# Kernel optimization log

Hardware: AMD Instinct MI355X
Metric: run time of the kernel (lower is better)

The kernel has to match this reference:

```python
import jax, jax.numpy as jnp
import numpy as np

TOKENS, IN_F, OUT_F = 65536, 1024, 1024


def setup_inputs() -> dict:
    key = jax.random.key(0)
    kx, kw = jax.random.split(key)
    x = jax.random.normal(kx, (TOKENS, IN_F), dtype=jnp.float32)
    weight = jax.random.normal(kw, (OUT_F, IN_F), dtype=jnp.float32) * 0.05
    return {"x": x, "weight": weight}


def reference(x, weight):
    # per-output-row scale: alpha = mean(|w|) over in_features
    alpha = jnp.mean(jnp.abs(weight), axis=1, keepdims=True)  # [out, 1]
    w_bin = jnp.sign(weight) * alpha                          # [out, in]
    # F.linear(x, w_bin) == x @ w_bin.T
    return jnp.einsum("ti,oi->to", x, w_bin)
```

## Files before the change

### kernel.cpp

```cpp
#include <hip/hip_runtime.h>


typedef _Float16 half8 __attribute__((ext_vector_type(8)));
typedef _Float16 half4v __attribute__((ext_vector_type(4)));
typedef float f32x4 __attribute__((ext_vector_type(4)));

#define TOKENS 65536
#define INF 1024
#define OUTF 1024
#define BM 256
#define BN 256
#define BK 32
#define NKT 32

__device__ __forceinline__ void gload_lds16(const void* g, void* l) {
  __builtin_amdgcn_global_load_lds(
      (const __attribute__((address_space(1))) unsigned int*)g,
      (__attribute__((address_space(3))) unsigned int*)l, 16, 0, 0);
}

__device__ __forceinline__ half8 cvt8(f32x4 a, f32x4 b) {
  half8 h;
  h[0] = (_Float16)a[0]; h[1] = (_Float16)a[1];
  h[2] = (_Float16)a[2]; h[3] = (_Float16)a[3];
  h[4] = (_Float16)b[0]; h[5] = (_Float16)b[1];
  h[6] = (_Float16)b[2]; h[7] = (_Float16)b[3];
  return h;
}

__global__ __launch_bounds__(256) void bl_prep(const float* __restrict__ w,
                                               _Float16* __restrict__ sbin,
                                               float* __restrict__ alpha) {
  const int o = blockIdx.x;
  const int tid = threadIdx.x;
  const float4 v = ((const float4*)(w + (size_t)o * INF))[tid];
  float s = fabsf(v.x) + fabsf(v.y) + fabsf(v.z) + fabsf(v.w);
  half4v h;
  h[0] = (_Float16)((v.x > 0.f) ? 1.f : ((v.x < 0.f) ? -1.f : 0.f));
  h[1] = (_Float16)((v.y > 0.f) ? 1.f : ((v.y < 0.f) ? -1.f : 0.f));
  h[2] = (_Float16)((v.z > 0.f) ? 1.f : ((v.z < 0.f) ? -1.f : 0.f));
  h[3] = (_Float16)((v.w > 0.f) ? 1.f : ((v.w < 0.f) ? -1.f : 0.f));
  *(half4v*)(sbin + (size_t)o * INF + tid * 4) = h;
#pragma unroll
  for (int off = 32; off > 0; off >>= 1) s += __shfl_down(s, off, 64);
  __shared__ float red[4];
  const int wave = tid >> 6, lane = tid & 63;
  if (lane == 0) red[wave] = s;
  __syncthreads();
  if (tid == 0) alpha[o] = (red[0] + red[1] + red[2] + red[3]) * (1.0f / 1024.0f);
}

__global__ __launch_bounds__(512, 2) void bl_gemm(const float* __restrict__ x,
                                                  const _Float16* __restrict__ sbin,
                                                  const float* __restrict__ alpha,
                                                  float* __restrict__ out) {
  __shared__ float ldsA[3][BM * BK];
  __shared__ _Float16 ldsB[3][BN * BK];

  const int tid = threadIdx.x;
  const int lane = tid & 63;
  const int wid = tid >> 6;
  const int l15 = lane & 15;
  const int kc = lane >> 4;
  const int wr = wid >> 1;
  const int wc = wid & 1;

  const int bid = blockIdx.x;
  const int wgid = (bid & 7) * 128 + (bid >> 3);
  const int bm0 = (wgid >> 2) * BM;
  const int bn0 = (wgid & 3) * BN;

  size_t aSrc[4];
  int aDst[4];
#pragma unroll
  for (int q = 0; q < 4; ++q) {
    const int ci = q * 512 + tid;
    const int row = ci >> 3;
    const int c = (ci & 7) ^ (row & 7);
    aSrc[q] = (size_t)(bm0 + row) * INF + c * 4;
    aDst[q] = ci * 16;
  }
  size_t bSrc[2];
  int bDst[2];
#pragma unroll
  for (int p = 0; p < 2; ++p) {
    const int ci = p * 512 + tid;
    const int row = ci >> 2;
    const int c = (ci & 3) ^ (row & 3);
    bSrc[p] = (size_t)(bn0 + row) * INF + c * 8;
    bDst[p] = ci * 16;
  }
  int aRd[4][2];
#pragma unroll
  for (int mf = 0; mf < 4; ++mf) {
    const int row = wr * 64 + mf * 16 + l15;
#pragma unroll
    for (int d = 0; d < 2; ++d)
      aRd[mf][d] = row * 128 + (((2 * kc + d) ^ (row & 7)) << 4);
  }
  int bRd[8];
#pragma unroll
  for (int nf = 0; nf < 8; ++nf) {
    const int row = wc * 128 + nf * 16 + l15;
    bRd[nf] = row * 64 + ((kc ^ (row & 3)) << 4);
  }

  f32x4 acc[4][8] = {};

#define STAGE(SB_, tk_)                                                        \
  {                                                                            \
    const size_t ko_ = (size_t)(tk_) * BK;                                     \
    gload_lds16(x + aSrc[0] + ko_, (char*)&ldsA[SB_][0] + aDst[0]);            \
    gload_lds16(x + aSrc[1] + ko_, (char*)&ldsA[SB_][0] + aDst[1]);            \
    gload_lds16(x + aSrc[2] + ko_, (char*)&ldsA[SB_][0] + aDst[2]);            \
    gload_lds16(x + aSrc[3] + ko_, (char*)&ldsA[SB_][0] + aDst[3]);            \
    gload_lds16(sbin + bSrc[0] + ko_, (char*)&ldsB[SB_][0] + bDst[0]);         \
    gload_lds16(sbin + bSrc[1] + ko_, (char*)&ldsB[SB_][0] + bDst[1]);         \
  }

#define COMPUTE(RB_)                                                           \
  {                                                                            \
    const char* pa_ = (const char*)&ldsA[RB_][0];                              \
    const char* pb_ = (const char*)&ldsB[RB_][0];                              \
    f32x4 lo0 = *(const f32x4*)(pa_ + aRd[0][0]);                              \
    f32x4 hi0 = *(const f32x4*)(pa_ + aRd[0][1]);                              \
    f32x4 lo1 = *(const f32x4*)(pa_ + aRd[1][0]);                              \
    f32x4 hi1 = *(const f32x4*)(pa_ + aRd[1][1]);                              \
    f32x4 lo2 = *(const f32x4*)(pa_ + aRd[2][0]);                              \
    f32x4 hi2 = *(const f32x4*)(pa_ + aRd[2][1]);                              \
    f32x4 lo3 = *(const f32x4*)(pa_ + aRd[3][0]);                              \
    f32x4 hi3 = *(const f32x4*)(pa_ + aRd[3][1]);                              \
    const half8 af0 = cvt8(lo0, hi0);                                          \
    const half8 af1 = cvt8(lo1, hi1);                                          \
    const half8 af2 = cvt8(lo2, hi2);                                          \
    const half8 af3 = cvt8(lo3, hi3);                                          \
    __builtin_amdgcn_s_setprio(1);                                             \
    _Pragma("unroll") for (int nf = 0; nf < 8; ++nf) {                         \
      const half8 b = *(const half8*)(pb_ + bRd[nf]);                          \
      acc[0][nf] = __builtin_amdgcn_mfma_f32_16x16x32_f16(af0, b, acc[0][nf], 0, 0, 0); \
      acc[1][nf] = __builtin_amdgcn_mfma_f32_16x16x32_f16(af1, b, acc[1][nf], 0, 0, 0); \
      acc[2][nf] = __builtin_amdgcn_mfma_f32_16x16x32_f16(af2, b, acc[2][nf], 0, 0, 0); \
      acc[3][nf] = __builtin_amdgcn_mfma_f32_16x16x32_f16(af3, b, acc[3][nf], 0, 0, 0); \
    }                                                                          \
    __builtin_amdgcn_s_setprio(0);                                             \
  }

#define PH(T_, RB_, SB_)                                                       \
  {                                                                            \
    STAGE(SB_, (T_) + 2);                                                      \
    COMPUTE(RB_);                                                              \
    asm volatile("s_waitcnt vmcnt(6)" ::: "memory");                           \
    __builtin_amdgcn_s_barrier();                                              \
  }

  STAGE(0, 0);
  STAGE(1, 1);
  asm volatile("s_waitcnt vmcnt(6)" ::: "memory");
  __builtin_amdgcn_s_barrier();

#pragma unroll 1
  for (int u = 0; u < 10; ++u) {
    PH(3 * u + 0, 0, 2)
    PH(3 * u + 1, 1, 0)
    PH(3 * u + 2, 2, 1)
  }
  COMPUTE(0);
  asm volatile("s_waitcnt vmcnt(0)" ::: "memory");
  __builtin_amdgcn_s_barrier();
  COMPUTE(1);

#undef PH
#undef COMPUTE
#undef STAGE

  float al[8];
#pragma unroll
  for (int n = 0; n < 8; ++n) al[n] = alpha[bn0 + wc * 128 + n * 16 + l15];
#pragma unroll
  for (int mf = 0; mf < 4; ++mf) {
    const int row0 = bm0 + wr * 64 + mf * 16 + kc * 4;
#pragma unroll
    for (int n = 0; n < 8; ++n) {
      const int col = bn0 + wc * 128 + n * 16 + l15;
#pragma unroll
      for (int j = 0; j < 4; ++j)
        out[(size_t)(row0 + j) * OUTF + col] = acc[mf][n][j] * al[n];
    }
  }
}

extern "C" void kernel_launch(void* const* d_in, const int* in_sizes, int n_in,
                              void* d_out, int out_size, void* d_ws, size_t ws_size,
                              hipStream_t stream) {
  const float* x = (const float*)d_in[0];
  const float* w = (const float*)d_in[1];
  float* out = (float*)d_out;
  _Float16* sbin = (_Float16*)d_ws;
  float* alpha = (float*)((char*)d_ws + (size_t)OUTF * INF * 2);

  bl_prep<<<dim3(OUTF), dim3(256), 0, stream>>>(w, sbin, alpha);
  bl_gemm<<<dim3((TOKENS / BM) * (OUTF / BN)), dim3(512), 0, stream>>>(x, sbin, alpha, out);
}
```

Measured before the change: 229.2 us.

## Pre-convert activations to fp16 in a separate pass and use fp16 GEMM

Adds a conversion kernel that writes x as fp16 into the workspace, then runs a new GEMM reading fp16 tiles with BK=64 and double buffering, removing per-tile fp32-to-fp16 conversion and halving LDS traffic for A. Falls back to a reworked fp32-input GEMM (two-stage buffering, adjusted B swizzle) when the workspace is too small. The extra pass adds a full read and write of the activation matrix through HBM.

```diff
diff --git a/kernel.cpp b/kernel.cpp
--- a/kernel.cpp
+++ b/kernel.cpp
@@ -10,8 +10,6 @@
 #define OUTF 1024
 #define BM 256
 #define BN 256
-#define BK 32
-#define NKT 32
 
 __device__ __forceinline__ void gload_lds16(const void* g, void* l) {
   __builtin_amdgcn_global_load_lds(
@@ -50,12 +48,23 @@
   if (tid == 0) alpha[o] = (red[0] + red[1] + red[2] + red[3]) * (1.0f / 1024.0f);
 }
 
-__global__ __launch_bounds__(512, 2) void bl_gemm(const float* __restrict__ x,
-                                                  const _Float16* __restrict__ sbin,
-                                                  const float* __restrict__ alpha,
-                                                  float* __restrict__ out) {
-  __shared__ float ldsA[3][BM * BK];
-  __shared__ _Float16 ldsB[3][BN * BK];
+__global__ __launch_bounds__(256) void bl_cvt(const float* __restrict__ x,
+                                              _Float16* __restrict__ x16) {
+  const size_t stride = (size_t)gridDim.x * 256 * 8;
+  for (size_t i = ((size_t)blockIdx.x * 256 + threadIdx.x) * 8;
+       i < (size_t)TOKENS * INF; i += stride) {
+    f32x4 v0 = *(const f32x4*)(x + i);
+    f32x4 v1 = *(const f32x4*)(x + i + 4);
+    *(half8*)(x16 + i) = cvt8(v0, v1);
+  }
+}
+
+__global__ __launch_bounds__(512) void bl_gemm16(const _Float16* __restrict__ x16,
+                                                 const _Float16* __restrict__ sbin,
+                                                 const float* __restrict__ alpha,
+                                                 float* __restrict__ out) {
+  __shared__ _Float16 ldsA[2][BM * 64];
+  __shared__ _Float16 ldsB[2][BN * 64];
 
   const int tid = threadIdx.x;
   const int lane = tid & 63;
@@ -70,24 +79,146 @@
   const int bm0 = (wgid >> 2) * BM;
   const int bn0 = (wgid & 3) * BN;
 
-  size_t aSrc[4];
-  int aDst[4];
+  int aSrc[4], bSrc[4];
+  int dst[4];
 #pragma unroll
   for (int q = 0; q < 4; ++q) {
     const int ci = q * 512 + tid;
     const int row = ci >> 3;
     const int c = (ci & 7) ^ (row & 7);
-    aSrc[q] = (size_t)(bm0 + row) * INF + c * 4;
+    aSrc[q] = (bm0 + row) * INF + c * 8;
+    bSrc[q] = (bn0 + row) * INF + c * 8;
+    dst[q] = ci * 16;
+  }
+  int slotKs[2];
+#pragma unroll
+  for (int ks = 0; ks < 2; ++ks) slotKs[ks] = (((ks * 4 + kc) ^ (l15 & 7)) << 4);
+  int aRd[4];
+#pragma unroll
+  for (int mf = 0; mf < 4; ++mf) aRd[mf] = (wr * 64 + mf * 16 + l15) * 128;
+  int bRd[8];
+#pragma unroll
+  for (int nf = 0; nf < 8; ++nf) bRd[nf] = (wc * 128 + nf * 16 + l15) * 128;
+
+  f32x4 acc[4][8] = {};
+
+#define STAGE(SB_, tk_)                                                        \
+  {                                                                            \
+    const int ko_ = (tk_)*64;                                                  \
+    gload_lds16(x16 + aSrc[0] + ko_, (char*)&ldsA[SB_][0] + dst[0]);           \
+    gload_lds16(x16 + aSrc[1] + ko_, (char*)&ldsA[SB_][0] + dst[1]);           \
+    gload_lds16(x16 + aSrc[2] + ko_, (char*)&ldsA[SB_][0] + dst[2]);           \
+    gload_lds16(x16 + aSrc[3] + ko_, (char*)&ldsA[SB_][0] + dst[3]);           \
+    gload_lds16(sbin + bSrc[0] + ko_, (char*)&ldsB[SB_][0] + dst[0]);          \
+    gload_lds16(sbin + bSrc[1] + ko_, (char*)&ldsB[SB_][0] + dst[1]);          \
+    gload_lds16(sbin + bSrc[2] + ko_, (char*)&ldsB[SB_][0] + dst[2]);          \
+    gload_lds16(sbin + bSrc[3] + ko_, (char*)&ldsB[SB_][0] + dst[3]);          \
+  }
+
+#define MF4(AC_, B_)                                                           \
+  acc[0][AC_] = __builtin_amdgcn_mfma_f32_16x16x32_f16(af0, B_, acc[0][AC_], 0, 0, 0); \
+  acc[1][AC_] = __builtin_amdgcn_mfma_f32_16x16x32_f16(af1, B_, acc[1][AC_], 0, 0, 0); \
+  acc[2][AC_] = __builtin_amdgcn_mfma_f32_16x16x32_f16(af2, B_, acc[2][AC_], 0, 0, 0); \
+  acc[3][AC_] = __builtin_amdgcn_mfma_f32_16x16x32_f16(af3, B_, acc[3][AC_], 0, 0, 0);
+
+#define KSLICE(RB_, KS_)                                                       \
+  {                                                                            \
+    const char* pa_ = (const char*)&ldsA[RB_][0];                              \
+    const char* pb_ = (const char*)&ldsB[RB_][0];                              \
+    const int sl_ = slotKs[KS_];                                               \
+    const half8 af0 = *(const half8*)(pa_ + aRd[0] + sl_);                     \
+    const half8 af1 = *(const half8*)(pa_ + aRd[1] + sl_);                     \
+    const half8 af2 = *(const half8*)(pa_ + aRd[2] + sl_);                     \
+    const half8 af3 = *(const half8*)(pa_ + aRd[3] + sl_);                     \
+    half8 b0 = *(const half8*)(pb_ + bRd[0] + sl_);                            \
+    half8 b1 = *(const half8*)(pb_ + bRd[1] + sl_);                            \
+    half8 b2 = *(const half8*)(pb_ + bRd[2] + sl_);                            \
+    half8 b3 = *(const half8*)(pb_ + bRd[3] + sl_);                            \
+    MF4(0, b0) MF4(1, b1) MF4(2, b2) MF4(3, b3)                                \
+    b0 = *(const half8*)(pb_ + bRd[4] + sl_);                                  \
+    b1 = *(const half8*)(pb_ + bRd[5] + sl_);                                  \
+    b2 = *(const half8*)(pb_ + bRd[6] + sl_);                                  \
+    b3 = *(const half8*)(pb_ + bRd[7] + sl_);                                  \
+    MF4(4, b0) MF4(5, b1) MF4(6, b2) MF4(7, b3)                                \
+  }
+
+#define COMPUTE(RB_)                                                           \
+  {                                                                            \
+    __builtin_amdgcn_s_setprio(1);                                             \
+    KSLICE(RB_, 0)                                                             \
+    KSLICE(RB_, 1)                                                             \
+    __builtin_amdgcn_s_setprio(0);                                             \
+  }
+
+  STAGE(0, 0);
+  __syncthreads();
+
+#pragma unroll 1
+  for (int u = 0; u < 8; ++u) {
+    STAGE(1, 2 * u + 1);
+    COMPUTE(0);
+    __syncthreads();
+    if (u < 7) STAGE(0, 2 * u + 2);
+    COMPUTE(1);
+    __syncthreads();
+  }
+#undef COMPUTE
+#undef KSLICE
+#undef MF4
+#undef STAGE
+
+  float al[8];
+#pragma unroll
+  for (int n = 0; n < 8; ++n) al[n] = alpha[bn0 + wc * 128 + n * 16 + l15];
+#pragma unroll
+  for (int mf = 0; mf < 4; ++mf) {
+    const int row0 = bm0 + wr * 64 + mf * 16 + kc * 4;
+#pragma unroll
+    for (int n = 0; n < 8; ++n) {
+      const int col = bn0 + wc * 128 + n * 16 + l15;
+#pragma unroll
+      for (int j = 0; j < 4; ++j)
+        out[(size_t)(row0 + j) * OUTF + col] = acc[mf][n][j] * al[n];
+    }
+  }
+}
+
+__global__ __launch_bounds__(512) void bl_gemm32(const float* __restrict__ x,
+                                                 const _Float16* __restrict__ sbin,
+                                                 const float* __restrict__ alpha,
+                                                 float* __restrict__ out) {
+  __shared__ float ldsA[2][BM * 32];
+  __shared__ _Float16 ldsB[2][BN * 32];
+
+  const int tid = threadIdx.x;
+  const int lane = tid & 63;
+  const int wid = tid >> 6;
+  const int l15 = lane & 15;
+  const int kc = lane >> 4;
+  const int wr = wid >> 1;
+  const int wc = wid & 1;
+
+  const int bid = blockIdx.x;
+  const int wgid = (bid & 7) * 128 + (bid >> 3);
+  const int bm0 = (wgid >> 2) * BM;
+  const int bn0 = (wgid & 3) * BN;
+
+  int aSrc[4], aDst[4];
+#pragma unroll
+  for (int q = 0; q < 4; ++q) {
+    const int ci = q * 512 + tid;
+    const int row = ci >> 3;
+    const int c = (ci & 7) ^ (row & 7);
+    aSrc[q] = (bm0 + row) * INF + c * 4;
     aDst[q] = ci * 16;
   }
-  size_t bSrc[2];
-  int bDst[2];
+  int bSrc[2], bDst[2];
 #pragma unroll
   for (int p = 0; p < 2; ++p) {
     const int ci = p * 512 + tid;
     const int row = ci >> 2;
-    const int c = (ci & 3) ^ (row & 3);
-    bSrc[p] = (size_t)(bn0 + row) * INF + c * 8;
+    const int c = (ci & 3) ^ ((row >> 1) & 3);
+    bSrc[p] = (bn0 + row) * INF + c * 8;
     bDst[p] = ci * 16;
   }
   int aRd[4][2];
@@ -102,14 +233,14 @@
 #pragma unroll
   for (int nf = 0; nf < 8; ++nf) {
     const int row = wc * 128 + nf * 16 + l15;
-    bRd[nf] = row * 64 + ((kc ^ (row & 3)) << 4);
+    bRd[nf] = row * 64 + ((kc ^ ((row >> 1) & 3)) << 4);
   }
 
   f32x4 acc[4][8] = {};
 
 #define STAGE(SB_, tk_)                                                        \
   {                                                                            \
-    const size_t ko_ = (size_t)(tk_) * BK;                                     \
+    const int ko_ = (tk_)*32;                                                  \
     gload_lds16(x + aSrc[0] + ko_, (char*)&ldsA[SB_][0] + aDst[0]);            \
     gload_lds16(x + aSrc[1] + ko_, (char*)&ldsA[SB_][0] + aDst[1]);            \
     gload_lds16(x + aSrc[2] + ko_, (char*)&ldsA[SB_][0] + aDst[2]);            \
@@ -118,6 +249,12 @@
     gload_lds16(sbin + bSrc[1] + ko_, (char*)&ldsB[SB_][0] + bDst[1]);         \
   }
 
+#define MF4(AC_, B_)                                                           \
+  acc[0][AC_] = __builtin_amdgcn_mfma_f32_16x16x32_f16(af0, B_, acc[0][AC_], 0, 0, 0); \
+  acc[1][AC_] = __builtin_amdgcn_mfma_f32_16x16x32_f16(af1, B_, acc[1][AC_], 0, 0, 0); \
+  acc[2][AC_] = __builtin_amdgcn_mfma_f32_16x16x32_f16(af2, B_, acc[2][AC_], 0, 0, 0); \
+  acc[3][AC_] = __builtin_amdgcn_mfma_f32_16x16x32_f16(af3, B_, acc[3][AC_], 0, 0, 0);
+
 #define COMPUTE(RB_)                                                           \
   {                                                                            \
     const char* pa_ = (const char*)&ldsA[RB_][0];                              \
@@ -126,51 +263,42 @@
     f32x4 hi0 = *(const f32x4*)(pa_ + aRd[0][1]);                              \
     f32x4 lo1 = *(const f32x4*)(pa_ + aRd[1][0]);                              \
     f32x4 hi1 = *(const f32x4*)(pa_ + aRd[1][1]);                              \
-    f32x4 lo2 = *(const f32x4*)(pa_ + aRd[2][0]);                              \
-    f32x4 hi2 = *(const f32x4*)(pa_ + aRd[2][1]);                              \
-    f32x4 lo3 = *(const f32x4*)(pa_ + aRd[3][0]);                              \
-    f32x4 hi3 = *(const f32x4*)(pa_ + aRd[3][1]);                              \
     const half8 af0 = cvt8(lo0, hi0);                                          \
     const half8 af1 = cvt8(lo1, hi1);                                          \
-    const half8 af2 = cvt8(lo2, hi2);                                          \
-    const half8 af3 = cvt8(lo3, hi3);                                          \
+    lo0 = *(const f32x4*)(pa_ + aRd[2][0]);                                    \
+    hi0 = *(const f32x4*)(pa_ + aRd[2][1]);                                    \
+    lo1 = *(const f32x4*)(pa_ + aRd[3][0]);                                    \
+    hi1 = *(const f32x4*)(pa_ + aRd[3][1]);                                    \
+    const half8 af2 = cvt8(lo0, hi0);                                          \
+    const half8 af3 = cvt8(lo1, hi1);                                          \
     __builtin_amdgcn_s_setprio(1);                                             \
-    _Pragma("unroll") for (int nf = 0; nf < 8; ++nf) {                         \
-      const half8 b = *(const half8*)(pb_ + bRd[nf]);                          \
-      acc[0][nf] = __builtin_amdgcn_mfma_f32_16x16x32_f16(af0, b, acc[0][nf], 0, 0, 0); \
-      acc[1][nf] = __builtin_amdgcn_mfma_f32_16x16x32_f16(af1, b, acc[1][nf], 0, 0, 0); \
-      acc[2][nf] = __builtin_amdgcn_mfma_f32_16x16x32_f16(af2, b, acc[2][nf], 0, 0, 0); \
-      acc[3][nf] = __builtin_amdgcn_mfma_f32_16x16x32_f16(af3, b, acc[3][nf], 0, 0, 0); \
-    }                                                                          \
+    half8 b0 = *(const half8*)(pb_ + bRd[0]);                                  \
+    half8 b1 = *(const half8*)(pb_ + bRd[1]);                                  \
+    half8 b2 = *(const half8*)(pb_ + bRd[2]);                                  \
+    half8 b3 = *(const half8*)(pb_ + bRd[3]);                                  \
+    MF4(0, b0) MF4(1, b1) MF4(2, b2) MF4(3, b3)                                \
+    b0 = *(const half8*)(pb_ + bRd[4]);                                        \
+    b1 = *(const half8*)(pb_ + bRd[5]);                                        \
+    b2 = *(const half8*)(pb_ + bRd[6]);                                        \
+    b3 = *(const half8*)(pb_ + bRd[7]);                                        \
+    MF4(4, b0) MF4(5, b1) MF4(6, b2) MF4(7, b3)                                \
     __builtin_amdgcn_s_setprio(0);                                             \
   }
 
-#define PH(T_, RB_, SB_)                                                       \
-  {                                                                            \
-    STAGE(SB_, (T_) + 2);                                                      \
-    COMPUTE(RB_);                                                              \
-    asm volatile("s_waitcnt vmcnt(6)" ::: "memory");                           \
-    __builtin_amdgcn_s_barrier();                                              \
-  }
-
   STAGE(0, 0);
-  STAGE(1, 1);
-  asm volatile("s_waitcnt vmcnt(6)" ::: "memory");
-  __builtin_amdgcn_s_barrier();
+  __syncthreads();
 
 #pragma unroll 1
-  for (int u = 0; u < 10; ++u) {
-    PH(3 * u + 0, 0, 2)
-    PH(3 * u + 1, 1, 0)
-    PH(3 * u + 2, 2, 1)
-  }
-  COMPUTE(0);
-  asm volatile("s_waitcnt vmcnt(0)" ::: "memory");
-  __builtin_amdgcn_s_barrier();
-  COMPUTE(1);
-
-#undef PH
+  for (int u = 0; u < 16; ++u) {
+    STAGE(1, 2 * u + 1);
+    COMPUTE(0);
+    __syncthreads();
+    if (u < 15) STAGE(0, 2 * u + 2);
+    COMPUTE(1);
+    __syncthreads();
+  }
 #undef COMPUTE
+#undef MF4
 #undef STAGE
 
   float al[8];
@@ -195,9 +323,22 @@
   const float* x = (const float*)d_in[0];
   const float* w = (const float*)d_in[1];
   float* out = (float*)d_out;
-  _Float16* sbin = (_Float16*)d_ws;
-  float* alpha = (float*)((char*)d_ws + (size_t)OUTF * INF * 2);
-
-  bl_prep<<<dim3(OUTF), dim3(256), 0, stream>>>(w, sbin, alpha);
-  bl_gemm<<<dim3((TOKENS / BM) * (OUTF / BN)), dim3(512), 0, stream>>>(x, sbin, alpha, out);
-}
+
+  const size_t x16_bytes = (size_t)TOKENS * INF * 2;
+  const size_t sbin_bytes = (size_t)OUTF * INF * 2;
+  const size_t needed = x16_bytes + sbin_bytes + OUTF * 4;
+
+  if (ws_size >= needed) {
+    _Float16* x16 = (_Float16*)d_ws;
+    _Float16* sbin = (_Float16*)((char*)d_ws + x16_bytes);
+    float* alpha = (float*)((char*)d_ws + x16_bytes + sbin_bytes);
+    bl_prep<<<dim3(OUTF), dim3(256), 0, stream>>>(w, sbin, alpha);
+    bl_cvt<<<dim3(2048), dim3(256), 0, stream>>>(x, x16);
+    bl_gemm16<<<dim3((TOKENS / BM) * (OUTF / BN)), dim3(512), 0, stream>>>(x16, sbin, alpha, out);
+  } else {
+    _Float16* sbin = (_Float16*)d_ws;
+    float* alpha = (float*)((char*)d_ws + sbin_bytes);
+    bl_prep<<<dim3(OUTF), dim3(256), 0, stream>>>(w, sbin, alpha);
+    bl_gemm32<<<dim3((TOKENS / BM) * (OUTF / BN)), dim3(512), 0, stream>>>(x, sbin, alpha, out);
+  }
+}
```

Result: slower. 276.2 us (+20.5%).
